# Kernel optimization log

Hardware: AMD Instinct MI355X
Metric: run time of the kernel (lower is better)

## Reference

```python
import jax, jax.numpy as jnp
import numpy as np
from jax import lax

N, C1, C2, H, W = 4, 256, 256, 80, 80
CH = 128           # c_ = int(c2 * e)
G, KS = 1, 3       # groups, kernel_size
K = KS * KS        # sampling points per group
PAD, DIL = 1, 1
EPS_BN, EPS_LN = 1e-5, 1e-6


def conv_bn_silu(x, w, g, b, m, v, stride=1):
    # ultralytics Conv: conv(bias=False) + BatchNorm2d(eval) + SiLU
    pad = (w.shape[2] - 1) // 2
    y = lax.conv_general_dilated(x, w, (stride, stride), [(pad, pad), (pad, pad)],
                                 dimension_numbers=('NCHW', 'OIHW', 'NCHW'))
    s = g / jnp.sqrt(v + EPS_BN)
    y = y * s[None, :, None, None] + (b - m * s)[None, :, None, None]
    return jax.nn.silu(y)


def dcnv3_core(x, offset, mask):
    # x: (N,H,W,C) NHWC; offset: (N,H,W,G*K*2); mask: (N,H,W,G,K) softmaxed over K
    n, h, w, c = x.shape
    gc = c // G
    xp = jnp.pad(x, ((0, 0), (PAD, PAD), (PAD, PAD), (0, 0)))
    Hp, Wp = h + 2 * PAD, w + 2 * PAD
    base = (DIL * (KS - 1)) // 2
    # reference points (normalized by padded spatial size), stride 1
    ref_x = (jnp.arange(w, dtype=x.dtype) + base + 0.5) / Wp   # (W,)
    ref_y = (jnp.arange(h, dtype=x.dtype) + base + 0.5) / Hp   # (H,)
    gx = (jnp.arange(KS, dtype=x.dtype) * DIL - base) / Wp
    gy = (jnp.arange(KS, dtype=x.dtype) * DIL - base) / Hp
    grid_x = jnp.repeat(gx, KS)   # point p = i*KS + j -> x = gx[i]
    grid_y = jnp.tile(gy, KS)     # y = gy[j]  (torch meshgrid 'ij' ordering)
    off = offset.reshape(n, h, w, G, K, 2)
    loc_x = ref_x[None, None, :, None, None] + grid_x + off[..., 0] / Wp
    loc_y = ref_y[None, :, None, None, None] + grid_y + off[..., 1] / Hp
    # grid_sample align_corners=False: pixel = norm * size - 0.5
    px = loc_x * Wp - 0.5
    py = loc_y * Hp - 0.5
    x0 = jnp.floor(px); y0 = jnp.floor(py)
    lw, lh = px - x0, py - y0
    x0i, y0i = x0.astype(jnp.int32), y0.astype(jnp.int32)
    xv = jnp.transpose(xp.reshape(n, Hp * Wp, G, gc), (0, 2, 1, 3))  # (N,G,S,gc)
    tw = lambda a: jnp.transpose(a, (0, 3, 1, 2, 4))[..., None]      # (N,H,W,G,K)->(N,G,H,W,K,1)

    def gather(yi, xi):
        valid = ((xi >= 0) & (xi < Wp) & (yi >= 0) & (yi < Hp)).astype(x.dtype)
        idx = jnp.clip(yi, 0, Hp - 1) * Wp + jnp.clip(xi, 0, Wp - 1)
        idx = jnp.transpose(idx, (0, 3, 1, 2, 4)).reshape(n, G, h * w * K)
        v = jnp.take_along_axis(xv, idx[..., None], axis=2).reshape(n, G, h, w, K, gc)
        return v * tw(valid)   # zeros padding_mode

    out = (gather(y0i, x0i) * tw((1 - lh) * (1 - lw))
           + gather(y0i, x0i + 1) * tw((1 - lh) * lw)
           + gather(y0i + 1, x0i) * tw(lh * (1 - lw))
           + gather(y0i + 1, x0i + 1) * tw(lh * lw))   # (N,G,H,W,K,gc)
    m = jnp.transpose(mask, (0, 3, 1, 2, 4))[..., None]
    out = (out * m).sum(axis=4)                        # (N,G,H,W,gc)
    return jnp.transpose(out, (0, 2, 3, 1, 4)).reshape(n, h, w, c)


def forward(x, w1, g1, b1, m1, v1, w2, g2, b2, m2, v2,
            dw_w, dw_b, ln_g, ln_b, off_w, off_b, msk_w, msk_b,
            in_w, in_b, out_w, out_b, g3, b3, m3, v3):
    y = conv_bn_silu(x, w1, g1, b1, m1, v1)   # cv1: 3x3 Conv c1->c_
    y = conv_bn_silu(y, w2, g2, b2, m2, v2)   # cv2.conv: 1x1 Conv c_->c2
    t = jnp.transpose(y, (0, 2, 3, 1))        # NHWC
    x_proj = t @ in_w.T + in_b                # input_proj
    # dw_conv: depthwise 3x3 -> LayerNorm (channels_last) -> GELU
    dw = lax.conv_general_dilated(y, dw_w, (1, 1), [(1, 1), (1, 1)],
                                  dimension_numbers=('NCHW', 'OIHW', 'NCHW'),
                                  feature_group_count=C2)
    dw = jnp.transpose(dw, (0, 2, 3, 1)) + dw_b
    mu = dw.mean(-1, keepdims=True)
    var = ((dw - mu) ** 2).mean(-1, keepdims=True)
    dw = (dw - mu) / jnp.sqrt(var + EPS_LN) * ln_g + ln_b
    dw = jax.nn.gelu(dw, approximate=False)
    offset = dw @ off_w.T + off_b                                       # (N,H,W,G*K*2)
    mask = jax.nn.softmax((dw @ msk_w.T + msk_b).reshape(N, H, W, G, K), axis=-1)
    z = dcnv3_core(x_proj, offset, mask)
    z = z @ out_w.T + out_b                   # output_proj
    z = jnp.transpose(z, (0, 3, 1, 2))        # NCHW
    s = g3 / jnp.sqrt(v3 + EPS_BN)
    z = z * s[None, :, None, None] + (b3 - m3 * s)[None, :, None, None]
    z = jax.nn.silu(z)
    return x + z                              # shortcut (c1 == c2)


def setup_inputs():
    key = jax.random.key(0)
    ks = jax.random.split(key, 16)
    r = lambda k, s, sc=0.05: jax.random.normal(k, s, dtype=jnp.float32) * sc
    return {
        'x': jax.random.normal(ks[0], (N, C1, H, W), dtype=jnp.float32),
        'w1': r(ks[1], (CH, C1, 3, 3)),
        'g1': jnp.ones((CH,), jnp.float32), 'b1': jnp.zeros((CH,), jnp.float32),
        'm1': r(ks[2], (CH,), 0.1),
        'v1': jax.random.uniform(ks[3], (CH,), jnp.float32, 0.5, 1.5),
        'w2': r(ks[4], (C2, CH, 1, 1)),
        'g2': jnp.ones((C2,), jnp.float32), 'b2': jnp.zeros((C2,), jnp.float32),
        'm2': r(ks[5], (C2,), 0.1),
        'v2': jax.random.uniform(ks[6], (C2,), jnp.float32, 0.5, 1.5),
        'dw_w': r(ks[7], (C2, 1, 3, 3)), 'dw_b': jnp.zeros((C2,), jnp.float32),
        'ln_g': jnp.ones((C2,), jnp.float32), 'ln_b': jnp.zeros((C2,), jnp.float32),
        'off_w': r(ks[8], (G * K * 2, C2), 0.01), 'off_b': jnp.zeros((G * K * 2,), jnp.float32),
        'msk_w': r(ks[9], (G * K, C2), 0.01), 'msk_b': jnp.zeros((G * K,), jnp.float32),
        'in_w': r(ks[10], (C2, C2)), 'in_b': jnp.zeros((C2,), jnp.float32),
        'out_w': r(ks[11], (C2, C2)), 'out_b': jnp.zeros((C2,), jnp.float32),
        'g3': jnp.ones((C2,), jnp.float32), 'b3': jnp.zeros((C2,), jnp.float32),
        'm3': r(ks[12], (C2,), 0.1),
        'v3': jax.random.uniform(ks[13], (C2,), jnp.float32, 0.5, 1.5),
    }


def reference(x, w1, g1, b1, m1, v1, w2, g2, b2, m2, v2,
              dw_w, dw_b, ln_g, ln_b, off_w, off_b, msk_w, msk_b,
              in_w, in_b, out_w, out_b, g3, b3, m3, v3):
    return forward(x, w1, g1, b1, m1, v1, w2, g2, b2, m2, v2,
                   dw_w, dw_b, ln_g, ln_b, off_w, off_b, msk_w, msk_b,
                   in_w, in_b, out_w, out_b, g3, b3, m3, v3)
```

## Files before the change

### kernel.cpp

```cpp
#include <hip/hip_runtime.h>
#include <cmath>

#define TN 4
#define TC1 256
#define TCH 128
#define TC2 256
#define TH 80
#define TW 80
#define THP 82
#define TWP 84
#define NPIX (TN*TH*TW)

#define OFF_WBF   0
#define OFF_W2B   294912
#define OFF_INWB  327680
#define OFF_OUTWB 393216
#define OFF_DWT   458752
#define OFF_WCAT  461056
#define OFF_WCATB 467968
#define OFF_T1    468128
#define OFF_T2    468512
#define OFF_T3P   469024
#define OFF_XPAD  469504
#define OFF_Y1B   3997696
#define OFF_Y1P   7525888
#define OFF_Y2N   7525888
#define OFF_DWN   469504
#define OFF_RAWN  10802688
#define OFF_ZN    11493888

typedef __attribute__((ext_vector_type(8))) short bf16x8;
typedef __attribute__((ext_vector_type(4))) float f32x4;

__device__ __forceinline__ float siluf(float v) { return v / (1.f + expf(-v)); }
__device__ __forceinline__ short rnbf(float f) {
  unsigned u = __float_as_uint(f);
  unsigned r = (u + 0x7fffu + ((u >> 16) & 1u)) >> 16;
  return (short)r;
}
__device__ __forceinline__ float bf2f(short s) {
  return __uint_as_float(((unsigned)(unsigned short)s) << 16);
}

__global__ __launch_bounds__(256) void k_prep(
    const float* __restrict__ w1, const float* __restrict__ g1, const float* __restrict__ b1,
    const float* __restrict__ m1, const float* __restrict__ v1,
    const float* __restrict__ w2, const float* __restrict__ g2, const float* __restrict__ b2,
    const float* __restrict__ m2, const float* __restrict__ v2,
    const float* __restrict__ dww, const float* __restrict__ offw, const float* __restrict__ offb,
    const float* __restrict__ mskw, const float* __restrict__ mskb,
    const float* __restrict__ inw, const float* __restrict__ outw, const float* __restrict__ outb,
    const float* __restrict__ g3, const float* __restrict__ b3,
    const float* __restrict__ m3, const float* __restrict__ v3,
    float* __restrict__ ws)
{
  int i = blockIdx.x * 256 + threadIdx.x;
  if (i < 294912) {
    int co = i / 2304; int r = i - co * 2304;
    int tap = r >> 8; int ci = r & 255; int ky = tap / 3; int kx = tap - ky * 3;
    float s = g1[co] * __frsqrt_rn(v1[co] + 1e-5f);
    ((short*)(ws + OFF_WBF))[i] = rnbf(w1[((co * TC1 + ci) * 3 + ky) * 3 + kx] * s);
    return;
  }
  i -= 294912;
  if (i < 32768) {
    int co = i >> 7; int ci = i & 127;
    float s = g2[co] * __frsqrt_rn(v2[co] + 1e-5f);
    ((short*)(ws + OFF_W2B))[i] = rnbf(w2[co * TCH + ci] * s);
    return;
  }
  i -= 32768;
  if (i < 65536) {
    int co = i >> 8; int ci = i & 255;
    ((short*)(ws + OFF_INWB))[i] = rnbf(inw[co * TC2 + ci]);
    return;
  }
  i -= 65536;
  if (i < 65536) {
    int co = i >> 8; int ci = i & 255;
    float s = g3[co] * __frsqrt_rn(v3[co] + 1e-5f);
    ((short*)(ws + OFF_OUTWB))[i] = rnbf(outw[co * TC2 + ci] * s);
    return;
  }
  i -= 65536;
  if (i < 2304) { int c = i & 255; int j = i >> 8; ws[OFF_DWT + i] = dww[c * 9 + j]; return; }
  i -= 2304;
  if (i < 8192) {
    int c = i & 255; int j = i >> 8;
    float v = 0.f;
    if (j < 18) v = offw[j * 256 + c];
    else if (j < 27) v = mskw[(j - 18) * 256 + c];
    ((short*)(ws + OFF_WCAT))[i] = rnbf(v);
    return;
  }
  i -= 8192;
  if (i < 27) { ws[OFF_WCATB + i] = (i < 18) ? offb[i] : mskb[i - 18]; return; }
  i -= 27;
  if (i < 128) { float s = g1[i] / sqrtf(v1[i] + 1e-5f); ws[OFF_T1 + i] = b1[i] - m1[i] * s; return; }
  i -= 128;
  if (i < 256) { float s = g2[i] / sqrtf(v2[i] + 1e-5f); ws[OFF_T2 + i] = b2[i] - m2[i] * s; return; }
  i -= 256;
  if (i < 256) { float s = g3[i] / sqrtf(v3[i] + 1e-5f); ws[OFF_T3P + i] = outb[i] * s + b3[i] - m3[i] * s; return; }
}

__global__ __launch_bounds__(256) void k_padx(const float* __restrict__ x, short* __restrict__ xpn)
{
  __shared__ short lds[80 * 40];
  int b = blockIdx.x;
  int cc = b & 7; int hp = (b >> 3) % THP; int n = b / (THP * 8);
  int c0 = cc * 32;
  int t = threadIdx.x;
  int h = hp - 1;
  bool hv = (h >= 0 && h < TH);
  if (hv) {
    for (int f = t; f < 640; f += 256) {
      int ci = f / 20; int w4 = (f - ci * 20) * 4;
      float4 xv = *(const float4*)(x + ((n * TC1 + c0 + ci) * TH + h) * TW + w4);
      lds[(w4 + 0) * 40 + ci] = rnbf(xv.x);
      lds[(w4 + 1) * 40 + ci] = rnbf(xv.y);
      lds[(w4 + 2) * 40 + ci] = rnbf(xv.z);
      lds[(w4 + 3) * 40 + ci] = rnbf(xv.w);
    }
  }
  __syncthreads();
  short* op = xpn + ((n * THP + hp) * TWP) * TC2 + c0;
  for (int g = t; g < 672; g += 256) {
    int ci4 = (g & 7) * 4; int wp = g >> 3;
    short4 v = {0, 0, 0, 0};
    if (hv && wp >= 1 && wp <= TW) v = *(const short4*)(&lds[(wp - 1) * 40 + ci4]);
    *(short4*)(op + wp * TC2 + ci4) = v;
  }
}

#define A_STR 40
__global__ __launch_bounds__(256) void k_cv1(const short* __restrict__ xpn, const short* __restrict__ wbf,
                                             float* __restrict__ y1p)
{
  __shared__ short As[2][128 * A_STR];
  __shared__ short Bs[2][128 * A_STR];

  int b = blockIdx.x;
  int wt = b % 5; b /= 5; int ht = b % 10; b /= 10; int n = b & 3; int ks = b >> 2;
  int w0 = wt * 16, h0 = ht * 8;
  int tap0 = ks * 3;

  int tid = threadIdx.x;
  int wave = tid >> 6, lane = tid & 63;
  int ln = lane & 15, q = lane >> 4;
  int cohalf = (wave & 1) * 64;
  int pxhalf = (wave >> 1) * 64;

  int srow = tid >> 1;
  int ssub = (tid & 1) * 16;
  int hr = srow >> 4, wc = srow & 15;
  const short* arow = wbf + srow * 2304 + ssub;
  const short* brow = xpn + ((n * THP + h0 + hr) * TWP + (w0 + wc)) * 256 + ssub;

  f32x4 acc[4][4];
#pragma unroll
  for (int i = 0; i < 4; ++i)
#pragma unroll
    for (int j = 0; j < 4; ++j) acc[i][j] = (f32x4){0.f, 0.f, 0.f, 0.f};

  bf16x8 ra0, ra1, rb0, rb1;

  auto grab = [&](int c) {
    int rt = c >> 3;
    int atap = tap0 + rt;
    int ci0 = (c & 7) * 32;
    int ky = atap / 3, kx = atap - ky * 3;
    const short* ap = arow + atap * 256 + ci0;
    const short* bp = brow + (ky * TWP + kx) * 256 + ci0;
    ra0 = *(const bf16x8*)(ap);
    ra1 = *(const bf16x8*)(ap + 8);
    rb0 = *(const bf16x8*)(bp);
    rb1 = *(const bf16x8*)(bp + 8);
  };
  auto put = [&](int buf) {
    int o = srow * A_STR + ssub;
    *(bf16x8*)(&As[buf][o])     = ra0;
    *(bf16x8*)(&As[buf][o + 8]) = ra1;
    *(bf16x8*)(&Bs[buf][o])     = rb0;
    *(bf16x8*)(&Bs[buf][o + 8]) = rb1;
  };
  auto comp = [&](int buf) {
    bf16x8 af[4], bfv[4];
#pragma unroll
    for (int mt = 0; mt < 4; ++mt)
      af[mt] = *(const bf16x8*)(&As[buf][(cohalf + mt * 16 + ln) * A_STR + q * 8]);
#pragma unroll
    for (int nt = 0; nt < 4; ++nt)
      bfv[nt] = *(const bf16x8*)(&Bs[buf][(pxhalf + nt * 16 + ln) * A_STR + q * 8]);
#pragma unroll
    for (int mt = 0; mt < 4; ++mt)
#pragma unroll
      for (int nt = 0; nt < 4; ++nt)
        acc[mt][nt] = __builtin_amdgcn_mfma_f32_16x16x32_bf16(af[mt], bfv[nt], acc[mt][nt], 0, 0, 0);
  };

  grab(0);
  put(0);
  __syncthreads();
  for (int c = 0; c < 24; ++c) {
    if (c < 23) grab(c + 1);
    comp(c & 1);
    if (c < 23) {
      __syncthreads();
      put((c + 1) & 1);
      __syncthreads();
    }
  }

  float* yp = y1p + ks * (NPIX * TCH);
#pragma unroll
  for (int mt = 0; mt < 4; ++mt)
#pragma unroll
    for (int nt = 0; nt < 4; ++nt) {
      int p = pxhalf + nt * 16 + ln;
      int pr = p >> 4, pc = p & 15;
      int pix = (n * TH + h0 + pr) * TW + (w0 + pc);
      int co = cohalf + mt * 16 + q * 4;
      *(f32x4*)(yp + pix * TCH + co) = acc[mt][nt];
    }
}

__global__ __launch_bounds__(256) void k_y1red(const float* __restrict__ y1p, const float* __restrict__ t1v,
                                               short* __restrict__ y1b)
{
  int i = blockIdx.x * 256 + threadIdx.x;
  int co4 = (i & 31) * 4;
  int pix = i >> 5;
  float4 a = *(const float4*)(y1p + pix * TCH + co4);
  float4 bq = *(const float4*)(y1p + NPIX * TCH + pix * TCH + co4);
  float4 cq = *(const float4*)(y1p + 2 * NPIX * TCH + pix * TCH + co4);
  float4 t = *(const float4*)(t1v + co4);
  short4 o;
  o.x = rnbf(siluf(a.x + bq.x + cq.x + t.x));
  o.y = rnbf(siluf(a.y + bq.y + cq.y + t.y));
  o.z = rnbf(siluf(a.z + bq.z + cq.z + t.z));
  o.w = rnbf(siluf(a.w + bq.w + cq.w + t.w));
  *(short4*)(y1b + pix * TCH + co4) = o;
}

__global__ __launch_bounds__(256) void k_cv2(const short* __restrict__ y1b, const short* __restrict__ w2b,
                                             const float* __restrict__ t2v, short* __restrict__ y2b)
{
  __shared__ short As[2][128 * A_STR];
  __shared__ short Bs[2][128 * A_STR];

  int b = blockIdx.x;
  int ch = b & 1; int pt = b >> 1;
  int co_base = ch * 128;
  int pix0 = pt * 128;

  int tid = threadIdx.x;
  int wave = tid >> 6, lane = tid & 63;
  int ln = lane & 15, q = lane >> 4;
  int coh = (wave & 1) * 64;
  int pxh = (wave >> 1) * 64;

  int srow = tid >> 1;
  int ssub = (tid & 1) * 16;
  const short* arow = w2b + (co_base + srow) * TCH + ssub;
  const short* brow = y1b + (pix0 + srow) * TCH + ssub;

  f32x4 acc[4][4];
#pragma unroll
  for (int i = 0; i < 4; ++i)
#pragma unroll
    for (int j = 0; j < 4; ++j) acc[i][j] = (f32x4){0.f, 0.f, 0.f, 0.f};

  bf16x8 ra0, ra1, rb0, rb1;
  auto grab = [&](int c) {
    const short* ap = arow + c * 32;
    const short* bp = brow + c * 32;
    ra0 = *(const bf16x8*)(ap);
    ra1 = *(const bf16x8*)(ap + 8);
    rb0 = *(const bf16x8*)(bp);
    rb1 = *(const bf16x8*)(bp + 8);
  };
  auto put = [&](int buf) {
    int o = srow * A_STR + ssub;
    *(bf16x8*)(&As[buf][o])     = ra0;
    *(bf16x8*)(&As[buf][o + 8]) = ra1;
    *(bf16x8*)(&Bs[buf][o])     = rb0;
    *(bf16x8*)(&Bs[buf][o + 8]) = rb1;
  };
  auto comp = [&](int buf) {
    bf16x8 af[4], bfv[4];
#pragma unroll
    for (int mt = 0; mt < 4; ++mt)
      af[mt] = *(const bf16x8*)(&As[buf][(coh + mt * 16 + ln) * A_STR + q * 8]);
#pragma unroll
    for (int nt = 0; nt < 4; ++nt)
      bfv[nt] = *(const bf16x8*)(&Bs[buf][(pxh + nt * 16 + ln) * A_STR + q * 8]);
#pragma unroll
    for (int mt = 0; mt < 4; ++mt)
#pragma unroll
      for (int nt = 0; nt < 4; ++nt)
        acc[mt][nt] = __builtin_amdgcn_mfma_f32_16x16x32_bf16(af[mt], bfv[nt], acc[mt][nt], 0, 0, 0);
  };

  const int NCH = TCH / 32;
  grab(0);
  put(0);
  __syncthreads();
  for (int c = 0; c < NCH; ++c) {
    if (c < NCH - 1) grab(c + 1);
    comp(c & 1);
    if (c < NCH - 1) {
      __syncthreads();
      put((c + 1) & 1);
      __syncthreads();
    }
  }

#pragma unroll
  for (int mt = 0; mt < 4; ++mt) {
    int co = co_base + coh + mt * 16 + q * 4;
    float t0 = t2v[co], t1 = t2v[co + 1], t2 = t2v[co + 2], t3 = t2v[co + 3];
#pragma unroll
    for (int nt = 0; nt < 4; ++nt) {
      int pix = pix0 + pxh + nt * 16 + ln;
      short4 p;
      p.x = rnbf(siluf(acc[mt][nt][0] + t0));
      p.y = rnbf(siluf(acc[mt][nt][1] + t1));
      p.z = rnbf(siluf(acc[mt][nt][2] + t2));
      p.w = rnbf(siluf(acc[mt][nt][3] + t3));
      *(short4*)(y2b + pix * TC2 + co) = p;
    }
  }
}

__global__ __launch_bounds__(256) void k_proj_in(const short* __restrict__ y2b, const short* __restrict__ inwb,
                                                 const float* __restrict__ inb, short* __restrict__ xproj)
{
  __shared__ short As[2][128 * A_STR];
  __shared__ short Bs[2][128 * A_STR];

  int b = blockIdx.x;
  int ch = b & 1; int pt = b >> 1;
  int co_base = ch * 128;
  int pix0 = pt * 128;

  int tid = threadIdx.x;
  int wave = tid >> 6, lane = tid & 63;
  int ln = lane & 15, q = lane >> 4;
  int coh = (wave & 1) * 64;
  int pxh = (wave >> 1) * 64;

  int srow = tid >> 1;
  int ssub = (tid & 1) * 16;
  const short* arow = inwb + (co_base + srow) * TC2 + ssub;
  const short* brow = y2b + (pix0 + srow) * TC2 + ssub;

  f32x4 acc[4][4];
#pragma unroll
  for (int i = 0; i < 4; ++i)
#pragma unroll
    for (int j = 0; j < 4; ++j) acc[i][j] = (f32x4){0.f, 0.f, 0.f, 0.f};

  bf16x8 ra0, ra1, rb0, rb1;
  auto grab = [&](int c) {
    const short* ap = arow + c * 32;
    const short* bp = brow + c * 32;
    ra0 = *(const bf16x8*)(ap);
    ra1 = *(const bf16x8*)(ap + 8);
    rb0 = *(const bf16x8*)(bp);
    rb1 = *(const bf16x8*)(bp + 8);
  };
  auto put = [&](int buf) {
    int o = srow * A_STR + ssub;
    *(bf16x8*)(&As[buf][o])     = ra0;
    *(bf16x8*)(&As[buf][o + 8]) = ra1;
    *(bf16x8*)(&Bs[buf][o])     = rb0;
    *(bf16x8*)(&Bs[buf][o + 8]) = rb1;
  };
  auto comp = [&](int buf) {
    bf16x8 af[4], bfv[4];
#pragma unroll
    for (int mt = 0; mt < 4; ++mt)
      af[mt] = *(const bf16x8*)(&As[buf][(coh + mt * 16 + ln) * A_STR + q * 8]);
#pragma unroll
    for (int nt = 0; nt < 4; ++nt)
      bfv[nt] = *(const bf16x8*)(&Bs[buf][(pxh + nt * 16 + ln) * A_STR + q * 8]);
#pragma unroll
    for (int mt = 0; mt < 4; ++mt)
#pragma unroll
      for (int nt = 0; nt < 4; ++nt)
        acc[mt][nt] = __builtin_amdgcn_mfma_f32_16x16x32_bf16(af[mt], bfv[nt], acc[mt][nt], 0, 0, 0);
  };

  const int NCH = TC2 / 32;
  grab(0);
  put(0);
  __syncthreads();
  for (int c = 0; c < NCH; ++c) {
    if (c < NCH - 1) grab(c + 1);
    comp(c & 1);
    if (c < NCH - 1) {
      __syncthreads();
      put((c + 1) & 1);
      __syncthreads();
    }
  }

#pragma unroll
  for (int mt = 0; mt < 4; ++mt) {
    int co = co_base + coh + mt * 16 + q * 4;
    float b0 = inb[co], b1 = inb[co + 1], b2 = inb[co + 2], b3 = inb[co + 3];
#pragma unroll
    for (int nt = 0; nt < 4; ++nt) {
      int pix = pix0 + pxh + nt * 16 + ln;
      short4 p;
      p.x = rnbf(acc[mt][nt][0] + b0);
      p.y = rnbf(acc[mt][nt][1] + b1);
      p.z = rnbf(acc[mt][nt][2] + b2);
      p.w = rnbf(acc[mt][nt][3] + b3);
      *(short4*)(xproj + pix * TC2 + co) = p;
    }
  }
}

__global__ __launch_bounds__(256) void k_dwln(const short* __restrict__ y2b, const float* __restrict__ dwt,
                                              const float* __restrict__ dwb, const float* __restrict__ lng,
                                              const float* __restrict__ lnb, short* __restrict__ dwo)
{
  int tid = threadIdx.x;
  int wave = tid >> 6, lane = tid & 63;
  int half = lane >> 5;
  int pix = blockIdx.x * 8 + wave * 2 + half;
  int w = pix % TW; int h = (pix / TW) % TH; int n = pix / (TH * TW);
  int c0 = (lane & 31) * 8;

  float v[8];
  {
    float4 b0 = *(const float4*)(dwb + c0);
    float4 b1 = *(const float4*)(dwb + c0 + 4);
    v[0] = b0.x; v[1] = b0.y; v[2] = b0.z; v[3] = b0.w;
    v[4] = b1.x; v[5] = b1.y; v[6] = b1.z; v[7] = b1.w;
  }
#pragma unroll
  for (int dy = 0; dy < 3; ++dy) {
#pragma unroll
    for (int dx = 0; dx < 3; ++dx) {
      int hh = h + dy - 1, ww = w + dx - 1;
      bool ok = (hh >= 0) & (hh < TH) & (ww >= 0) & (ww < TW);
      int off = ok ? (((n * TH + hh) * TW + ww) * TC2 + c0) : c0;
      bf16x8 yv = *(const bf16x8*)(y2b + off);
      float m = ok ? 1.f : 0.f;
      const float* wp = dwt + (dy * 3 + dx) * TC2 + c0;
      float4 w0 = *(const float4*)(wp);
      float4 w1 = *(const float4*)(wp + 4);
      v[0] += bf2f(yv[0]) * w0.x * m;
      v[1] += bf2f(yv[1]) * w0.y * m;
      v[2] += bf2f(yv[2]) * w0.z * m;
      v[3] += bf2f(yv[3]) * w0.w * m;
      v[4] += bf2f(yv[4]) * w1.x * m;
      v[5] += bf2f(yv[5]) * w1.y * m;
      v[6] += bf2f(yv[6]) * w1.z * m;
      v[7] += bf2f(yv[7]) * w1.w * m;
    }
  }
  float sv = 0.f, sq = 0.f;
#pragma unroll
  for (int i = 0; i < 8; ++i) { sv += v[i]; sq += v[i] * v[i]; }
#pragma unroll
  for (int o = 16; o > 0; o >>= 1) { sv += __shfl_xor(sv, o); sq += __shfl_xor(sq, o); }
  float mu = sv * (1.f / 256.f);
  float var = sq * (1.f / 256.f) - mu * mu;
  float rs = 1.f / sqrtf(var + 1e-6f);
  float4 g0 = *(const float4*)(lng + c0);
  float4 g1 = *(const float4*)(lng + c0 + 4);
  float4 bb0 = *(const float4*)(lnb + c0);
  float4 bb1 = *(const float4*)(lnb + c0 + 4);
  float gv[8] = {g0.x, g0.y, g0.z, g0.w, g1.x, g1.y, g1.z, g1.w};
  float bv[8] = {bb0.x, bb0.y, bb0.z, bb0.w, bb1.x, bb1.y, bb1.z, bb1.w};
  const float is2 = 0.70710678118654752f;
  bf16x8 o8;
#pragma unroll
  for (int i = 0; i < 8; ++i) {
    float nv = (v[i] - mu) * rs * gv[i] + bv[i];
    o8[i] = rnbf(0.5f * nv * (1.f + erff(nv * is2)));
  }
  *(bf16x8*)(dwo + pix * TC2 + c0) = o8;
}

__global__ __launch_bounds__(256) void k_offmask(const short* __restrict__ dwo, const short* __restrict__ wcatb16,
                                                 const float* __restrict__ wcatb, float* __restrict__ raw)
{
  int tid = threadIdx.x;
  int wave = tid >> 6, lane = tid & 63;
  int ln = lane & 15, q = lane >> 4;
  int pix0 = blockIdx.x * 64 + wave * 16;

  f32x4 acc0 = {0.f, 0.f, 0.f, 0.f};
  f32x4 acc1 = acc0;

  const short* a0p = wcatb16 + ln * 256 + q * 8;
  const short* a1p = wcatb16 + (16 + ln) * 256 + q * 8;
  const short* bp  = dwo + (pix0 + ln) * 256 + q * 8;
#pragma unroll
  for (int kk = 0; kk < 256; kk += 32) {
    bf16x8 bf = *(const bf16x8*)(bp + kk);
    bf16x8 a0 = *(const bf16x8*)(a0p + kk);
    bf16x8 a1 = *(const bf16x8*)(a1p + kk);
    acc0 = __builtin_amdgcn_mfma_f32_16x16x32_bf16(a0, bf, acc0, 0, 0, 0);
    acc1 = __builtin_amdgcn_mfma_f32_16x16x32_bf16(a1, bf, acc1, 0, 0, 0);
  }

  int pix = pix0 + ln;
#pragma unroll
  for (int r = 0; r < 4; ++r) {
    int j0 = q * 4 + r;
    raw[pix * 27 + j0] = acc0[r] + wcatb[j0];
    int j1 = 16 + j0;
    if (j1 < 27) raw[pix * 27 + j1] = acc1[r] + wcatb[j1];
  }
}

__global__ __launch_bounds__(256) void k_dcn(const short* __restrict__ xproj, const float* __restrict__ raw,
                                             short* __restrict__ z)
{
  __shared__ int2 sp[8][36];
  int tid = threadIdx.x;
  int pixbase = blockIdx.x * 8;

  for (int j = tid; j < 288; j += 256) {
    int pxl = j / 36, t = j - pxl * 36;
    int pix = pixbase + pxl;
    int w = pix % TW; int h = (pix / TW) % TH;
    const float* r = raw + pix * 27;
    int k = t >> 2, tap = t & 3;
    int tx = tap & 1, ty = tap >> 1;
    float mx = r[18];
#pragma unroll
    for (int kk = 1; kk < 9; ++kk) mx = fmaxf(mx, r[18 + kk]);
    float sum = 0.f, ek = 0.f;
#pragma unroll
    for (int kk = 0; kk < 9; ++kk) {
      float ee = expf(r[18 + kk] - mx);
      sum += ee;
      if (kk == k) ek = ee;
    }
    float mk = ek / sum;
    float px = (float)(w + k / 3) + r[2 * k];
    float py = (float)(h + k % 3) + r[2 * k + 1];
    float x0f = floorf(px), y0f = floorf(py);
    float lw = px - x0f, lh = py - y0f;
    int x0 = (int)x0f + tx, y0 = (int)y0f + ty;
    float wt = mk * (tx ? lw : 1.f - lw) * (ty ? lh : 1.f - lh);
    bool valid = (x0 >= 1) & (x0 <= TW) & (y0 >= 1) & (y0 <= TH);
    int2 pr;
    pr.x = valid ? (((y0 - 1) * TW + (x0 - 1)) * TC2) : 0;
    pr.y = valid ? __float_as_int(wt) : 0;
    sp[pxl][t] = pr;
  }
  __syncthreads();

  int wave = tid >> 6, lane = tid & 63;
  int half = lane >> 5;
  int pxl = wave * 2 + half;
  int pix = pixbase + pxl;
  int n = pix / (TH * TW);
  int c0 = (lane & 31) * 8;
  const short* xb = xproj + n * (TH * TW * TC2) + c0;

  float a[8] = {0.f, 0.f, 0.f, 0.f, 0.f, 0.f, 0.f, 0.f};
#pragma unroll
  for (int t = 0; t < 36; ++t) {
    int2 pr = sp[pxl][t];
    float wt = __int_as_float(pr.y);
    bf16x8 v = *(const bf16x8*)(xb + pr.x);
#pragma unroll
    for (int i = 0; i < 8; ++i) a[i] += wt * bf2f(v[i]);
  }
  bf16x8 o8;
#pragma unroll
  for (int i = 0; i < 8; ++i) o8[i] = rnbf(a[i]);
  *(bf16x8*)(z + pix * TC2 + c0) = o8;
}

__global__ __launch_bounds__(256) void k_proj_out(const short* __restrict__ zb, const short* __restrict__ outwb,
                                                  const float* __restrict__ t3p,
                                                  const float* __restrict__ x, float* __restrict__ out)
{
  __shared__ short As[2][128 * A_STR];
  __shared__ short Bs[2][128 * A_STR];

  int b = blockIdx.x;
  int ch = b & 1; int pt = b >> 1;
  int co_base = ch * 128;
  int pix0 = pt * 128;

  int tid = threadIdx.x;
  int wave = tid >> 6, lane = tid & 63;
  int ln = lane & 15, q = lane >> 4;
  int coh = (wave & 1) * 64;
  int pxh = (wave >> 1) * 64;

  int srow = tid >> 1;
  int ssub = (tid & 1) * 16;
  const short* arow = outwb + (co_base + srow) * TC2 + ssub;
  const short* brow = zb + (pix0 + srow) * TC2 + ssub;

  f32x4 acc[4][4];
#pragma unroll
  for (int i = 0; i < 4; ++i)
#pragma unroll
    for (int j = 0; j < 4; ++j) acc[i][j] = (f32x4){0.f, 0.f, 0.f, 0.f};

  bf16x8 ra0, ra1, rb0, rb1;
  auto grab = [&](int c) {
    const short* ap = arow + c * 32;
    const short* bp = brow + c * 32;
    ra0 = *(const bf16x8*)(ap);
    ra1 = *(const bf16x8*)(ap + 8);
    rb0 = *(const bf16x8*)(bp);
    rb1 = *(const bf16x8*)(bp + 8);
  };
  auto put = [&](int buf) {
    int o = srow * A_STR + ssub;
    *(bf16x8*)(&As[buf][o])     = ra0;
    *(bf16x8*)(&As[buf][o + 8]) = ra1;
    *(bf16x8*)(&Bs[buf][o])     = rb0;
    *(bf16x8*)(&Bs[buf][o + 8]) = rb1;
  };
  auto comp = [&](int buf) {
    bf16x8 af[4], bfv[4];
#pragma unroll
    for (int mt = 0; mt < 4; ++mt)
      af[mt] = *(const bf16x8*)(&As[buf][(coh + mt * 16 + ln) * A_STR + q * 8]);
#pragma unroll
    for (int nt = 0; nt < 4; ++nt)
      bfv[nt] = *(const bf16x8*)(&Bs[buf][(pxh + nt * 16 + ln) * A_STR + q * 8]);
#pragma unroll
    for (int mt = 0; mt < 4; ++mt)
#pragma unroll
      for (int nt = 0; nt < 4; ++nt)
        acc[mt][nt] = __builtin_amdgcn_mfma_f32_16x16x32_bf16(af[mt], bfv[nt], acc[mt][nt], 0, 0, 0);
  };

  const int NCH = TC2 / 32;
  grab(0);
  put(0);
  __syncthreads();
  for (int c = 0; c < NCH; ++c) {
    if (c < NCH - 1) grab(c + 1);
    comp(c & 1);
    if (c < NCH - 1) {
      __syncthreads();
      put((c + 1) & 1);
      __syncthreads();
    }
  }

#pragma unroll
  for (int mt = 0; mt < 4; ++mt) {
    int co = co_base + coh + mt * 16 + q * 4;
#pragma unroll
    for (int nt = 0; nt < 4; ++nt) {
      int pix = pix0 + pxh + nt * 16 + ln;
      int n = pix / (TH * TW);
      int hw = pix - n * (TH * TW);
#pragma unroll
      for (int r = 0; r < 4; ++r) {
        int addr = (n * TC2 + co + r) * (TH * TW) + hw;
        out[addr] = x[addr] + siluf(acc[mt][nt][r] + t3p[co + r]);
      }
    }
  }
}

extern "C" void kernel_launch(void* const* d_in, const int* in_sizes, int n_in,
                              void* d_out, int out_size, void* d_ws, size_t ws_size,
                              hipStream_t stream)
{
  const float* x    = (const float*)d_in[0];
  const float* w1   = (const float*)d_in[1];
  const float* g1   = (const float*)d_in[2];
  const float* b1   = (const float*)d_in[3];
  const float* m1   = (const float*)d_in[4];
  const float* v1   = (const float*)d_in[5];
  const float* w2   = (const float*)d_in[6];
  const float* g2   = (const float*)d_in[7];
  const float* b2   = (const float*)d_in[8];
  const float* m2   = (const float*)d_in[9];
  const float* v2   = (const float*)d_in[10];
  const float* dww  = (const float*)d_in[11];
  const float* dwb  = (const float*)d_in[12];
  const float* lng  = (const float*)d_in[13];
  const float* lnb  = (const float*)d_in[14];
  const float* offw = (const float*)d_in[15];
  const float* offb = (const float*)d_in[16];
  const float* mskw = (const float*)d_in[17];
  const float* mskb = (const float*)d_in[18];
  const float* inw  = (const float*)d_in[19];
  const float* inb  = (const float*)d_in[20];
  const float* outw = (const float*)d_in[21];
  const float* outb = (const float*)d_in[22];
  const float* g3   = (const float*)d_in[23];
  const float* b3   = (const float*)d_in[24];
  const float* m3   = (const float*)d_in[25];
  const float* v3   = (const float*)d_in[26];

  float* ws  = (float*)d_ws;
  float* out = (float*)d_out;

  short* xpn    = (short*)(ws + OFF_XPAD);
  short* wbf    = (short*)(ws + OFF_WBF);
  short* w2b    = (short*)(ws + OFF_W2B);
  short* inwb   = (short*)(ws + OFF_INWB);
  short* outwb  = (short*)(ws + OFF_OUTWB);
  short* wcat16 = (short*)(ws + OFF_WCAT);
  float* y1p    = ws + OFF_Y1P;
  short* y1b    = (short*)(ws + OFF_Y1B);
  short* y2b    = (short*)(ws + OFF_Y2N);
  short* dwo    = (short*)(ws + OFF_DWN);
  float* raw    = ws + OFF_RAWN;
  short* zb     = (short*)(ws + OFF_ZN);
  short* xproj  = (short*)d_out;

  hipLaunchKernelGGL(k_prep, dim3(1836), dim3(256), 0, stream,
                     w1, g1, b1, m1, v1, w2, g2, b2, m2, v2,
                     dww, offw, offb, mskw, mskb, inw, outw, outb, g3, b3, m3, v3, ws);
  hipLaunchKernelGGL(k_padx,     dim3(TN * THP * 8), dim3(256), 0, stream, x, xpn);
  hipLaunchKernelGGL(k_cv1,      dim3(600),   dim3(256), 0, stream, xpn, wbf, y1p);
  hipLaunchKernelGGL(k_y1red,    dim3(3200),  dim3(256), 0, stream, y1p, ws + OFF_T1, y1b);
  hipLaunchKernelGGL(k_cv2,      dim3(400),   dim3(256), 0, stream, y1b, w2b, ws + OFF_T2, y2b);
  hipLaunchKernelGGL(k_proj_in,  dim3(400),   dim3(256), 0, stream, y2b, inwb, inb, xproj);
  hipLaunchKernelGGL(k_dwln,     dim3(3200),  dim3(256), 0, stream, y2b, ws + OFF_DWT, dwb, lng, lnb, dwo);
  hipLaunchKernelGGL(k_offmask,  dim3(400),   dim3(256), 0, stream, dwo, wcat16, ws + OFF_WCATB, raw);
  hipLaunchKernelGGL(k_dcn,      dim3(3200),  dim3(256), 0, stream, xproj, raw, zb);
  hipLaunchKernelGGL(k_proj_out, dim3(400),   dim3(256), 0, stream, zb, outwb, ws + OFF_T3P, x, out);
}
```

Baseline: 276.4 us.

## Fuse cv1 split-K partials and reduction into single GEMM with fused epilogue

Replaces the split-K cv1 GEMM, which wrote three fp32 partial buffers, and the separate reduce/SiLU kernel with one kernel. It iterates over all taps and applies bias, SiLU and bf16 rounding in the epilogue. The pixel tile is halved to 64 so the grid stays at 400 blocks. This removes the large fp32 partial write and read-back plus one launch, at the cost of a smaller tile, lower per-block reuse and longer serial K loops.

```diff
diff --git a/kernel.cpp b/kernel.cpp
--- a/kernel.cpp
+++ b/kernel.cpp
@@ -23,7 +23,6 @@
 #define OFF_T3P   469024
 #define OFF_XPAD  469504
 #define OFF_Y1B   3997696
-#define OFF_Y1P   7525888
 #define OFF_Y2N   7525888
 #define OFF_DWN   469504
 #define OFF_RAWN  10802688
@@ -133,113 +132,98 @@
 }
 
 #define A_STR 40
-__global__ __launch_bounds__(256) void k_cv1(const short* __restrict__ xpn, const short* __restrict__ wbf,
-                                             float* __restrict__ y1p)
+__global__ __launch_bounds__(256) void k_cv1f(const short* __restrict__ xpn, const short* __restrict__ wbf,
+                                              const float* __restrict__ t1v, short* __restrict__ y1b)
 {
   __shared__ short As[2][128 * A_STR];
-  __shared__ short Bs[2][128 * A_STR];
+  __shared__ short Bs[2][64 * A_STR];
 
   int b = blockIdx.x;
-  int wt = b % 5; b /= 5; int ht = b % 10; b /= 10; int n = b & 3; int ks = b >> 2;
-  int w0 = wt * 16, h0 = ht * 8;
-  int tap0 = ks * 3;
+  int wt = b % 5; b /= 5; int ht = b % 20; int n = b / 20;
+  int w0 = wt * 16, h0 = ht * 4;
 
   int tid = threadIdx.x;
   int wave = tid >> 6, lane = tid & 63;
   int ln = lane & 15, q = lane >> 4;
-  int cohalf = (wave & 1) * 64;
-  int pxhalf = (wave >> 1) * 64;
-
-  int srow = tid >> 1;
-  int ssub = (tid & 1) * 16;
-  int hr = srow >> 4, wc = srow & 15;
-  const short* arow = wbf + srow * 2304 + ssub;
-  const short* brow = xpn + ((n * THP + h0 + hr) * TWP + (w0 + wc)) * 256 + ssub;
-
-  f32x4 acc[4][4];
+  int coh = (wave & 1) * 64;
+  int pxh = (wave >> 1) * 32;
+
+  int arow = tid >> 1;
+  int asub = (tid & 1) * 16;
+  const short* abase = wbf + arow * 2304 + asub;
+  int brow_r = tid >> 2;
+  int bsub = (tid & 3) * 8;
+  int bhr = brow_r >> 4, bwc = brow_r & 15;
+  const short* bbase = xpn + ((n * THP + h0 + bhr) * TWP + (w0 + bwc)) * 256 + bsub;
+
+  f32x4 acc[4][2];
 #pragma unroll
   for (int i = 0; i < 4; ++i)
 #pragma unroll
-    for (int j = 0; j < 4; ++j) acc[i][j] = (f32x4){0.f, 0.f, 0.f, 0.f};
-
-  bf16x8 ra0, ra1, rb0, rb1;
-
+    for (int j = 0; j < 2; ++j) acc[i][j] = (f32x4){0.f, 0.f, 0.f, 0.f};
+
+  bf16x8 ra0, ra1, rb;
   auto grab = [&](int c) {
-    int rt = c >> 3;
-    int atap = tap0 + rt;
+    int tap = c >> 3;
     int ci0 = (c & 7) * 32;
-    int ky = atap / 3, kx = atap - ky * 3;
-    const short* ap = arow + atap * 256 + ci0;
-    const short* bp = brow + (ky * TWP + kx) * 256 + ci0;
+    int ky = tap / 3, kx = tap - ky * 3;
+    const short* ap = abase + tap * 256 + ci0;
+    const short* bp = bbase + (ky * TWP + kx) * 256 + ci0;
     ra0 = *(const bf16x8*)(ap);
     ra1 = *(const bf16x8*)(ap + 8);
-    rb0 = *(const bf16x8*)(bp);
-    rb1 = *(const bf16x8*)(bp + 8);
+    rb  = *(const bf16x8*)(bp);
   };
   auto put = [&](int buf) {
-    int o = srow * A_STR + ssub;
-    *(bf16x8*)(&As[buf][o])     = ra0;
-    *(bf16x8*)(&As[buf][o + 8]) = ra1;
-    *(bf16x8*)(&Bs[buf][o])     = rb0;
-    *(bf16x8*)(&Bs[buf][o + 8]) = rb1;
+    int oa = arow * A_STR + asub;
+    *(bf16x8*)(&As[buf][oa])     = ra0;
+    *(bf16x8*)(&As[buf][oa + 8]) = ra1;
+    *(bf16x8*)(&Bs[buf][brow_r * A_STR + bsub]) = rb;
   };
   auto comp = [&](int buf) {
-    bf16x8 af[4], bfv[4];
+    bf16x8 af[4], bfv[2];
 #pragma unroll
     for (int mt = 0; mt < 4; ++mt)
-      af[mt] = *(const bf16x8*)(&As[buf][(cohalf + mt * 16 + ln) * A_STR + q * 8]);
-#pragma unroll
-    for (int nt = 0; nt < 4; ++nt)
-      bfv[nt] = *(const bf16x8*)(&Bs[buf][(pxhalf + nt * 16 + ln) * A_STR + q * 8]);
+      af[mt] = *(const bf16x8*)(&As[buf][(coh + mt * 16 + ln) * A_STR + q * 8]);
+#pragma unroll
+    for (int nt = 0; nt < 2; ++nt)
+      bfv[nt] = *(const bf16x8*)(&Bs[buf][(pxh + nt * 16 + ln) * A_STR + q * 8]);
 #pragma unroll
     for (int mt = 0; mt < 4; ++mt)
 #pragma unroll
-      for (int nt = 0; nt < 4; ++nt)
+      for (int nt = 0; nt < 2; ++nt)
         acc[mt][nt] = __builtin_amdgcn_mfma_f32_16x16x32_bf16(af[mt], bfv[nt], acc[mt][nt], 0, 0, 0);
   };
 
   grab(0);
   put(0);
   __syncthreads();
-  for (int c = 0; c < 24; ++c) {
-    if (c < 23) grab(c + 1);
+  for (int c = 0; c < 72; ++c) {
+    if (c < 71) grab(c + 1);
     comp(c & 1);
-    if (c < 23) {
+    if (c < 71) {
       __syncthreads();
       put((c + 1) & 1);
       __syncthreads();
     }
   }
 
-  float* yp = y1p + ks * (NPIX * TCH);
-#pragma unroll
-  for (int mt = 0; mt < 4; ++mt)
-#pragma unroll
-    for (int nt = 0; nt < 4; ++nt) {
-      int p = pxhalf + nt * 16 + ln;
-      int pr = p >> 4, pc = p & 15;
-      int pix = (n * TH + h0 + pr) * TW + (w0 + pc);
-      int co = cohalf + mt * 16 + q * 4;
-      *(f32x4*)(yp + pix * TCH + co) = acc[mt][nt];
-    }
-}
-
-__global__ __launch_bounds__(256) void k_y1red(const float* __restrict__ y1p, const float* __restrict__ t1v,
-                                               short* __restrict__ y1b)
-{
-  int i = blockIdx.x * 256 + threadIdx.x;
-  int co4 = (i & 31) * 4;
-  int pix = i >> 5;
-  float4 a = *(const float4*)(y1p + pix * TCH + co4);
-  float4 bq = *(const float4*)(y1p + NPIX * TCH + pix * TCH + co4);
-  float4 cq = *(const float4*)(y1p + 2 * NPIX * TCH + pix * TCH + co4);
-  float4 t = *(const float4*)(t1v + co4);
-  short4 o;
-  o.x = rnbf(siluf(a.x + bq.x + cq.x + t.x));
-  o.y = rnbf(siluf(a.y + bq.y + cq.y + t.y));
-  o.z = rnbf(siluf(a.z + bq.z + cq.z + t.z));
-  o.w = rnbf(siluf(a.w + bq.w + cq.w + t.w));
-  *(short4*)(y1b + pix * TCH + co4) = o;
+#pragma unroll
+  for (int mt = 0; mt < 4; ++mt) {
+    int co = coh + mt * 16 + q * 4;
+    float t0 = t1v[co], t1 = t1v[co + 1], t2 = t1v[co + 2], t3 = t1v[co + 3];
+#pragma unroll
+    for (int nt = 0; nt < 2; ++nt) {
+      int pl = pxh + nt * 16 + ln;
+      int hr = pl >> 4, wc = pl & 15;
+      int pix = (n * TH + h0 + hr) * TW + (w0 + wc);
+      short4 p;
+      p.x = rnbf(siluf(acc[mt][nt][0] + t0));
+      p.y = rnbf(siluf(acc[mt][nt][1] + t1));
+      p.z = rnbf(siluf(acc[mt][nt][2] + t2));
+      p.w = rnbf(siluf(acc[mt][nt][3] + t3));
+      *(short4*)(y1b + pix * TCH + co) = p;
+    }
+  }
 }
 
 __global__ __launch_bounds__(256) void k_cv2(const short* __restrict__ y1b, const short* __restrict__ w2b,
@@ -713,7 +697,6 @@
   short* inwb   = (short*)(ws + OFF_INWB);
   short* outwb  = (short*)(ws + OFF_OUTWB);
   short* wcat16 = (short*)(ws + OFF_WCAT);
-  float* y1p    = ws + OFF_Y1P;
   short* y1b    = (short*)(ws + OFF_Y1B);
   short* y2b    = (short*)(ws + OFF_Y2N);
   short* dwo    = (short*)(ws + OFF_DWN);
@@ -725,8 +708,7 @@
                      w1, g1, b1, m1, v1, w2, g2, b2, m2, v2,
                      dww, offw, offb, mskw, mskb, inw, outw, outb, g3, b3, m3, v3, ws);
   hipLaunchKernelGGL(k_padx,     dim3(TN * THP * 8), dim3(256), 0, stream, x, xpn);
-  hipLaunchKernelGGL(k_cv1,      dim3(600),   dim3(256), 0, stream, xpn, wbf, y1p);
-  hipLaunchKernelGGL(k_y1red,    dim3(3200),  dim3(256), 0, stream, y1p, ws + OFF_T1, y1b);
+  hipLaunchKernelGGL(k_cv1f,     dim3(400),   dim3(256), 0, stream, xpn, wbf, ws + OFF_T1, y1b);
   hipLaunchKernelGGL(k_cv2,      dim3(400),   dim3(256), 0, stream, y1b, w2b, ws + OFF_T2, y2b);
   hipLaunchKernelGGL(k_proj_in,  dim3(400),   dim3(256), 0, stream, y2b, inwb, inb, xproj);
   hipLaunchKernelGGL(k_dwln,     dim3(3200),  dim3(256), 0, stream, y2b, ws + OFF_DWT, dwb, lng, lnb, dwo);
```

Result: no change. 278.2 us (+0.7%).

## Fuse cv1 split-K reduction into GEMM epilogue and coalesce proj_out stores via LDS

Applied to the files above, without the earlier changes.

The cv1 implicit GEMM no longer splits its 9 taps into three K-partitions that write fp32 partials. Each block now runs all 72 K-chunks and applies the BN shift, SiLU and bf16 rounding in its epilogue, which removes the k_y1red kernel and the fp32 partial round trip through memory. The trade-off is that the grid shrinks from 600 to 200 blocks, which may underfill the GPU's compute units. Separately, the proj_out epilogue transposes accumulators through LDS so that NCHW output and residual accesses are coalesced along pixels instead of strided scalar accesses.

```diff
diff --git a/kernel.cpp b/kernel.cpp
--- a/kernel.cpp
+++ b/kernel.cpp
@@ -23,7 +23,6 @@
 #define OFF_T3P   469024
 #define OFF_XPAD  469504
 #define OFF_Y1B   3997696
-#define OFF_Y1P   7525888
 #define OFF_Y2N   7525888
 #define OFF_DWN   469504
 #define OFF_RAWN  10802688
@@ -133,28 +132,27 @@
 }
 
 #define A_STR 40
-__global__ __launch_bounds__(256) void k_cv1(const short* __restrict__ xpn, const short* __restrict__ wbf,
-                                             float* __restrict__ y1p)
+__global__ __launch_bounds__(256) void k_cv1f(const short* __restrict__ xpn, const short* __restrict__ wbf,
+                                              const float* __restrict__ t1v, short* __restrict__ y1b)
 {
   __shared__ short As[2][128 * A_STR];
   __shared__ short Bs[2][128 * A_STR];
 
   int b = blockIdx.x;
-  int wt = b % 5; b /= 5; int ht = b % 10; b /= 10; int n = b & 3; int ks = b >> 2;
+  int wt = b % 5; b /= 5; int ht = b % 10; int n = b / 10;
   int w0 = wt * 16, h0 = ht * 8;
-  int tap0 = ks * 3;
 
   int tid = threadIdx.x;
   int wave = tid >> 6, lane = tid & 63;
   int ln = lane & 15, q = lane >> 4;
-  int cohalf = (wave & 1) * 64;
-  int pxhalf = (wave >> 1) * 64;
+  int coh = (wave & 1) * 64;
+  int pxh = (wave >> 1) * 64;
 
   int srow = tid >> 1;
   int ssub = (tid & 1) * 16;
-  int hr = srow >> 4, wc = srow & 15;
   const short* arow = wbf + srow * 2304 + ssub;
-  const short* brow = xpn + ((n * THP + h0 + hr) * TWP + (w0 + wc)) * 256 + ssub;
+  int bhr = srow >> 4, bwc = srow & 15;
+  const short* brow = xpn + ((n * THP + h0 + bhr) * TWP + (w0 + bwc)) * 256 + ssub;
 
   f32x4 acc[4][4];
 #pragma unroll
@@ -163,13 +161,11 @@
     for (int j = 0; j < 4; ++j) acc[i][j] = (f32x4){0.f, 0.f, 0.f, 0.f};
 
   bf16x8 ra0, ra1, rb0, rb1;
-
   auto grab = [&](int c) {
-    int rt = c >> 3;
-    int atap = tap0 + rt;
+    int tap = c >> 3;
     int ci0 = (c & 7) * 32;
-    int ky = atap / 3, kx = atap - ky * 3;
-    const short* ap = arow + atap * 256 + ci0;
+    int ky = tap / 3, kx = tap - (tap / 3) * 3;
+    const short* ap = arow + tap * 256 + ci0;
     const short* bp = brow + (ky * TWP + kx) * 256 + ci0;
     ra0 = *(const bf16x8*)(ap);
     ra1 = *(const bf16x8*)(ap + 8);
@@ -187,10 +183,10 @@
     bf16x8 af[4], bfv[4];
 #pragma unroll
     for (int mt = 0; mt < 4; ++mt)
-      af[mt] = *(const bf16x8*)(&As[buf][(cohalf + mt * 16 + ln) * A_STR + q * 8]);
+      af[mt] = *(const bf16x8*)(&As[buf][(coh + mt * 16 + ln) * A_STR + q * 8]);
 #pragma unroll
     for (int nt = 0; nt < 4; ++nt)
-      bfv[nt] = *(const bf16x8*)(&Bs[buf][(pxhalf + nt * 16 + ln) * A_STR + q * 8]);
+      bfv[nt] = *(const bf16x8*)(&Bs[buf][(pxh + nt * 16 + ln) * A_STR + q * 8]);
 #pragma unroll
     for (int mt = 0; mt < 4; ++mt)
 #pragma unroll
@@ -198,48 +194,37 @@
         acc[mt][nt] = __builtin_amdgcn_mfma_f32_16x16x32_bf16(af[mt], bfv[nt], acc[mt][nt], 0, 0, 0);
   };
 
+  const int NK = 72;
   grab(0);
   put(0);
   __syncthreads();
-  for (int c = 0; c < 24; ++c) {
-    if (c < 23) grab(c + 1);
+  for (int c = 0; c < NK; ++c) {
+    if (c < NK - 1) grab(c + 1);
     comp(c & 1);
-    if (c < 23) {
+    if (c < NK - 1) {
       __syncthreads();
       put((c + 1) & 1);
       __syncthreads();
     }
   }
 
-  float* yp = y1p + ks * (NPIX * TCH);
-#pragma unroll
-  for (int mt = 0; mt < 4; ++mt)
+#pragma unroll
+  for (int mt = 0; mt < 4; ++mt) {
+    int co = coh + mt * 16 + q * 4;
+    float t0 = t1v[co], t1 = t1v[co + 1], t2 = t1v[co + 2], t3 = t1v[co + 3];
 #pragma unroll
     for (int nt = 0; nt < 4; ++nt) {
-      int p = pxhalf + nt * 16 + ln;
-      int pr = p >> 4, pc = p & 15;
-      int pix = (n * TH + h0 + pr) * TW + (w0 + pc);
-      int co = cohalf + mt * 16 + q * 4;
-      *(f32x4*)(yp + pix * TCH + co) = acc[mt][nt];
-    }
-}
-
-__global__ __launch_bounds__(256) void k_y1red(const float* __restrict__ y1p, const float* __restrict__ t1v,
-                                               short* __restrict__ y1b)
-{
-  int i = blockIdx.x * 256 + threadIdx.x;
-  int co4 = (i & 31) * 4;
-  int pix = i >> 5;
-  float4 a = *(const float4*)(y1p + pix * TCH + co4);
-  float4 bq = *(const float4*)(y1p + NPIX * TCH + pix * TCH + co4);
-  float4 cq = *(const float4*)(y1p + 2 * NPIX * TCH + pix * TCH + co4);
-  float4 t = *(const float4*)(t1v + co4);
-  short4 o;
-  o.x = rnbf(siluf(a.x + bq.x + cq.x + t.x));
-  o.y = rnbf(siluf(a.y + bq.y + cq.y + t.y));
-  o.z = rnbf(siluf(a.z + bq.z + cq.z + t.z));
-  o.w = rnbf(siluf(a.w + bq.w + cq.w + t.w));
-  *(short4*)(y1b + pix * TCH + co4) = o;
+      int p = pxh + nt * 16 + ln;
+      int hr = p >> 4, wc = p & 15;
+      int pix = (n * TH + h0 + hr) * TW + (w0 + wc);
+      short4 o;
+      o.x = rnbf(siluf(acc[mt][nt][0] + t0));
+      o.y = rnbf(siluf(acc[mt][nt][1] + t1));
+      o.z = rnbf(siluf(acc[mt][nt][2] + t2));
+      o.w = rnbf(siluf(acc[mt][nt][3] + t3));
+      *(short4*)(y1b + pix * TCH + co) = o;
+    }
+  }
 }
 
 __global__ __launch_bounds__(256) void k_cv2(const short* __restrict__ y1b, const short* __restrict__ w2b,
@@ -655,19 +640,26 @@
     }
   }
 
+  __syncthreads();
+  float* tb = (float*)(&As[0][0]);
+  float* wb = tb + wave * 1056;
+  int pixw = pix0 + pxh;
+  int nn = pixw / (TH * TW);
+  int hw0 = pixw - nn * (TH * TW);
+
 #pragma unroll
   for (int mt = 0; mt < 4; ++mt) {
-    int co = co_base + coh + mt * 16 + q * 4;
-#pragma unroll
-    for (int nt = 0; nt < 4; ++nt) {
-      int pix = pix0 + pxh + nt * 16 + ln;
-      int n = pix / (TH * TW);
-      int hw = pix - n * (TH * TW);
-#pragma unroll
-      for (int r = 0; r < 4; ++r) {
-        int addr = (n * TC2 + co + r) * (TH * TW) + hw;
-        out[addr] = x[addr] + siluf(acc[mt][nt][r] + t3p[co + r]);
-      }
+#pragma unroll
+    for (int nt = 0; nt < 4; ++nt)
+#pragma unroll
+      for (int r = 0; r < 4; ++r)
+        wb[(q * 4 + r) * 66 + nt * 16 + ln] = acc[mt][nt][r];
+    int co = co_base + coh + mt * 16;
+#pragma unroll
+    for (int cl = 0; cl < 16; ++cl) {
+      float vv = wb[cl * 66 + lane];
+      int addr = (nn * TC2 + co + cl) * (TH * TW) + hw0 + lane;
+      out[addr] = x[addr] + siluf(vv + t3p[co + cl]);
     }
   }
 }
@@ -713,7 +705,6 @@
   short* inwb   = (short*)(ws + OFF_INWB);
   short* outwb  = (short*)(ws + OFF_OUTWB);
   short* wcat16 = (short*)(ws + OFF_WCAT);
-  float* y1p    = ws + OFF_Y1P;
   short* y1b    = (short*)(ws + OFF_Y1B);
   short* y2b    = (short*)(ws + OFF_Y2N);
   short* dwo    = (short*)(ws + OFF_DWN);
@@ -725,8 +716,7 @@
                      w1, g1, b1, m1, v1, w2, g2, b2, m2, v2,
                      dww, offw, offb, mskw, mskb, inw, outw, outb, g3, b3, m3, v3, ws);
   hipLaunchKernelGGL(k_padx,     dim3(TN * THP * 8), dim3(256), 0, stream, x, xpn);
-  hipLaunchKernelGGL(k_cv1,      dim3(600),   dim3(256), 0, stream, xpn, wbf, y1p);
-  hipLaunchKernelGGL(k_y1red,    dim3(3200),  dim3(256), 0, stream, y1p, ws + OFF_T1, y1b);
+  hipLaunchKernelGGL(k_cv1f,     dim3(200),   dim3(256), 0, stream, xpn, wbf, ws + OFF_T1, y1b);
   hipLaunchKernelGGL(k_cv2,      dim3(400),   dim3(256), 0, stream, y1b, w2b, ws + OFF_T2, y2b);
   hipLaunchKernelGGL(k_proj_in,  dim3(400),   dim3(256), 0, stream, y2b, inwb, inb, xproj);
   hipLaunchKernelGGL(k_dwln,     dim3(3200),  dim3(256), 0, stream, y2b, ws + OFF_DWT, dwb, lng, lnb, dwo);
```

Result: slower. 285.9 us (+3.4%).
